# Performance work log

Measured on AMD Instinct MI355X. Metric: run time of the kernel, lower is better.

Reference implementation:

```python
import jax, jax.numpy as jnp
import numpy as np

B, D, T = 8, 256, 8192
N_Q, BINS = 8, 1024
COMMIT_W = 0.25

def setup_inputs() -> dict:
    key = jax.random.key(0)
    k1, k2 = jax.random.split(key)
    x = jax.random.normal(k1, (B, D, T), dtype=jnp.float32)
    codebooks = jax.random.normal(k2, (N_Q, BINS, D), dtype=jnp.float32)
    return {"x": x, "sample_rate": 16000, "codebooks": codebooks}

def _rvq(x_btd, codebooks):
    # x_btd: [B, T, D]; codebooks: [n_q, bins, D]
    def step(residual, cb):
        # nearest codebook entry under squared euclidean distance
        dots = jnp.einsum('btd,kd->btk', residual, cb)          # [B, T, K]
        cb_sq = jnp.sum(cb * cb, axis=-1)                        # [K]
        dist = cb_sq[None, None, :] - 2.0 * dots                 # argmin-equivalent distance
        idx = jnp.argmin(dist, axis=-1)                          # [B, T] int32
        q = cb[idx]                                              # [B, T, D] gather
        # commitment loss (codebook side detached, EnCodec style)
        loss = COMMIT_W * jnp.mean((jax.lax.stop_gradient(q) - residual) ** 2)
        # straight-through estimator
        q_ste = residual + jax.lax.stop_gradient(q - residual)
        return residual - q_ste, (q_ste, idx, loss)

    _, (qs, codes, losses) = jax.lax.scan(step, x_btd, codebooks)
    quantized = jnp.sum(qs, axis=0)                              # [B, T, D]
    return quantized, codes, losses

def reference(x, sample_rate, codebooks):
    n_q = codebooks.shape[0]
    bins = codebooks.shape[1]
    x_btd = jnp.transpose(x, (0, 2, 1))                          # [B, T, D]
    quantized_btd, codes, losses = _rvq(x_btd, codebooks)
    quantized = jnp.transpose(quantized_btd, (0, 2, 1))          # [B, D, T]
    bw_per_q = np.log2(bins) * sample_rate / 1000.0
    bw = jnp.asarray(n_q * bw_per_q, dtype=x.dtype)
    commit_loss = jnp.mean(losses)
    return quantized, codes, bw, commit_loss
```

## Files before the change

kernel.cpp:

```cpp
#include <hip/hip_runtime.h>
#include <math.h>

typedef _Float16 f16;
typedef f16 f16x8 __attribute__((ext_vector_type(8)));
typedef float f32x4 __attribute__((ext_vector_type(4)));

#define B_ 8
#define D_ 256
#define T_ 8192
#define NQ 8
#define KB 1024
#define TT 64
#define NTHR 512

#define OUT_CODES (B_ * D_ * T_)
#define OUT_BW (OUT_CODES + NQ * B_ * T_)
#define OUT_LOSS (OUT_BW + 1)

#define R_BYTES 65536
#define RED_OFF R_BYTES
#define REDI_OFF (RED_OFF + 2048)
#define WSUM_OFF (REDI_OFF + 2048)
#define LDS_TOTAL (WSUM_OFF + 32)

#define WS_HI (8192 * 4)
#define CBW_HALVES (NQ * 8 * KB * 32)
#define WS_LO (WS_HI + CBW_HALVES * 2)

#define MFMA16(a, b, c) __builtin_amdgcn_mfma_f32_16x16x32_f16(a, b, c, 0, 0, 0)

__global__ void init_cbsq_kernel(const float* __restrict__ cb, const int* __restrict__ sr,
                                 float* __restrict__ csq, float* __restrict__ out) {
    int gid = blockIdx.x * blockDim.x + threadIdx.x;
    int row = gid >> 6;
    int lane = gid & 63;
    float4 v = ((const float4*)(cb + (size_t)row * D_))[lane];
    float s = fmaf(v.x, v.x, fmaf(v.y, v.y, fmaf(v.z, v.z, v.w * v.w)));
#pragma unroll
    for (int off = 32; off; off >>= 1) s += __shfl_down(s, off);
    if (lane == 0) csq[row] = s;
    if (gid == 0) {
        out[OUT_BW] = (float)(*sr) * (80.0f / 1000.0f);
        out[OUT_LOSS] = 0.0f;
    }
}

__global__ void init_split_kernel(const float* __restrict__ cb, f16* __restrict__ whi,
                                  f16* __restrict__ wlo) {
    int gid = blockIdx.x * 256 + threadIdx.x;
    int qdc = gid >> 10, k = gid & 1023;
    int q = qdc >> 3, dc = qdc & 7;
    const float* src = cb + ((size_t)(q * 1024 + k)) * 256 + dc * 32;
    size_t wo = (size_t)gid * 32;
#pragma unroll
    for (int jj = 0; jj < 4; ++jj) {
        float4 a = ((const float4*)src)[jj * 2];
        float4 c = ((const float4*)src)[jj * 2 + 1];
        float vals[8] = {a.x, a.y, a.z, a.w, c.x, c.y, c.z, c.w};
        f16x8 hv, lv;
#pragma unroll
        for (int i = 0; i < 8; ++i) {
            f16 h = (f16)vals[i];
            hv[i] = h;
            lv[i] = (f16)(vals[i] - (float)h);
        }
        *(f16x8*)&whi[wo + jj * 8] = hv;
        *(f16x8*)&wlo[wo + jj * 8] = lv;
    }
}

extern "C" __global__ __launch_bounds__(NTHR, 4)
void rvq_kernel(const float* __restrict__ x, const float* __restrict__ cb,
                const float* __restrict__ csq, const f16* __restrict__ whi,
                const f16* __restrict__ wlo, float* __restrict__ out) {
    extern __shared__ char smem[];
    f16* rs = (f16*)smem;
    float* redv = (float*)(smem + RED_OFF);
    int* redi = (int*)(smem + REDI_OFF);
    float* wsum = (float*)(smem + WSUM_OFF);

    const int tid = threadIdx.x;
    const int w = tid >> 6;
    const int l = tid & 63;
    const int l15 = l & 15;
    const int q4 = l >> 4;

    const int b = blockIdx.x >> 7;
    const int t0 = (blockIdx.x & 127) * TT;
    const float* xb = x + (size_t)b * D_ * T_;

    for (int d = tid >> 6; d < D_; d += 8) {
        float v = xb[(size_t)d * T_ + t0 + l];
        f16 h = (f16)v;
        const int sw = l & 7;
        rs[l * 512 + (((d >> 3) ^ sw) << 3) + (d & 7)] = h;
        rs[l * 512 + ((((d >> 3) + 32) ^ sw) << 3) + (d & 7)] = (f16)(v - (float)h);
    }

    float ssq = 0.0f;

    const f16* a_base = rs + l15 * 512;
    const int swA = l15 & 7;

    for (int q = 0; q < NQ; ++q) {
        const float* cbq = cb + (size_t)q * KB * D_;
        const char* wq = (const char*)(whi + (size_t)q * 8 * KB * 32);
        const char* lq = (const char*)(wlo + (size_t)q * 8 * KB * 32);

        __syncthreads();

        float bval[16];
        unsigned bidxp[8];
#pragma unroll
        for (int e = 0; e < 16; ++e) bval[e] = INFINITY;
#pragma unroll
        for (int p = 0; p < 8; ++p) bidxp[p] = 0;

#pragma unroll 1
        for (int s = 0; s < 4; ++s) {
            const int code0 = s * 256 + w * 32 + l15;
            const int vb0 = (code0 << 6) + q4 * 16;

            f32x4 ah[4][2];
#pragma unroll
            for (int mt = 0; mt < 4; ++mt)
#pragma unroll
                for (int nt = 0; nt < 2; ++nt) ah[mt][nt] = (f32x4)0.0f;

            f16x8 sa0h, sa0l, sa1h, sa1l;
            f16x8 sb0h, sb0l, sb1h, sb1l;

#define LOADSET(p0h, p0l, p1h, p1l, dcv) { \
            const char* wd_ = wq + (dcv) * 65536; \
            const char* ld_ = lq + (dcv) * 65536; \
            p0h = *(const f16x8*)(wd_ + vb0); \
            p0l = *(const f16x8*)(ld_ + vb0); \
            p1h = *(const f16x8*)(wd_ + vb0 + 1024); \
            p1l = *(const f16x8*)(ld_ + vb0 + 1024); }

#define STEP(dcv, c0h, c0l, c1h, c1l) { \
            const int ga_ = (dcv) * 4 + q4; \
            const int o1_ = (ga_ ^ swA) << 3; \
            const int o2_ = ((ga_ + 32) ^ swA) << 3; \
            f16x8 afa1 = *(const f16x8*)&a_base[o1_]; \
            f16x8 afa2 = *(const f16x8*)&a_base[o2_]; \
            f16x8 afb1 = *(const f16x8*)&a_base[8192 + o1_]; \
            f16x8 afb2 = *(const f16x8*)&a_base[8192 + o2_]; \
            __builtin_amdgcn_s_setprio(1); \
            ah[0][0] = MFMA16(afa1, c0h, ah[0][0]); \
            ah[0][0] = MFMA16(afa2, c0h, ah[0][0]); \
            ah[0][0] = MFMA16(afa1, c0l, ah[0][0]); \
            ah[0][1] = MFMA16(afa1, c1h, ah[0][1]); \
            ah[0][1] = MFMA16(afa2, c1h, ah[0][1]); \
            ah[0][1] = MFMA16(afa1, c1l, ah[0][1]); \
            __builtin_amdgcn_sched_barrier(0); \
            afa1 = *(const f16x8*)&a_base[16384 + o1_]; \
            afa2 = *(const f16x8*)&a_base[16384 + o2_]; \
            ah[1][0] = MFMA16(afb1, c0h, ah[1][0]); \
            ah[1][0] = MFMA16(afb2, c0h, ah[1][0]); \
            ah[1][0] = MFMA16(afb1, c0l, ah[1][0]); \
            ah[1][1] = MFMA16(afb1, c1h, ah[1][1]); \
            ah[1][1] = MFMA16(afb2, c1h, ah[1][1]); \
            ah[1][1] = MFMA16(afb1, c1l, ah[1][1]); \
            __builtin_amdgcn_sched_barrier(0); \
            afb1 = *(const f16x8*)&a_base[24576 + o1_]; \
            afb2 = *(const f16x8*)&a_base[24576 + o2_]; \
            ah[2][0] = MFMA16(afa1, c0h, ah[2][0]); \
            ah[2][0] = MFMA16(afa2, c0h, ah[2][0]); \
            ah[2][0] = MFMA16(afa1, c0l, ah[2][0]); \
            ah[2][1] = MFMA16(afa1, c1h, ah[2][1]); \
            ah[2][1] = MFMA16(afa2, c1h, ah[2][1]); \
            ah[2][1] = MFMA16(afa1, c1l, ah[2][1]); \
            __builtin_amdgcn_sched_barrier(0); \
            ah[3][0] = MFMA16(afb1, c0h, ah[3][0]); \
            ah[3][0] = MFMA16(afb2, c0h, ah[3][0]); \
            ah[3][0] = MFMA16(afb1, c0l, ah[3][0]); \
            ah[3][1] = MFMA16(afb1, c1h, ah[3][1]); \
            ah[3][1] = MFMA16(afb2, c1h, ah[3][1]); \
            ah[3][1] = MFMA16(afb1, c1l, ah[3][1]); \
            __builtin_amdgcn_s_setprio(0); \
            __builtin_amdgcn_sched_barrier(0); }

            LOADSET(sa0h, sa0l, sa1h, sa1l, 0)
            LOADSET(sb0h, sb0l, sb1h, sb1l, 1)
#pragma unroll 1
            for (int dc2 = 0; dc2 < 6; dc2 += 2) {
                STEP(dc2, sa0h, sa0l, sa1h, sa1l)
                LOADSET(sa0h, sa0l, sa1h, sa1l, dc2 + 2)
                STEP(dc2 + 1, sb0h, sb0l, sb1h, sb1l)
                LOADSET(sb0h, sb0l, sb1h, sb1l, dc2 + 3)
            }
            STEP(6, sa0h, sa0l, sa1h, sa1l)
            STEP(7, sb0h, sb0l, sb1h, sb1l)
#undef LOADSET
#undef STEP

            const float cq0 = csq[q * KB + code0];
            const float cq1 = csq[q * KB + code0 + 16];
#pragma unroll
            for (int nt = 0; nt < 2; ++nt) {
                const int code = code0 + nt * 16;
                const float cq = nt ? cq1 : cq0;
#pragma unroll
                for (int mt = 0; mt < 4; ++mt)
#pragma unroll
                    for (int rg = 0; rg < 4; ++rg) {
                        const int e = mt * 4 + rg;
                        const float dist = fmaf(-2.0f, ah[mt][nt][rg], cq);
                        if (dist < bval[e]) {
                            bval[e] = dist;
                            const int sh = (e & 1) * 16;
                            bidxp[e >> 1] = (bidxp[e >> 1] & ~(0xFFFFu << sh)) |
                                            ((unsigned)code << sh);
                        }
                    }
            }
        }
#pragma unroll
        for (int m = 1; m < 16; m <<= 1) {
#pragma unroll
            for (int p = 0; p < 8; ++p) {
                const unsigned op = __shfl_xor((int)bidxp[p], m);
#pragma unroll
                for (int h = 0; h < 2; ++h) {
                    const int e = p * 2 + h;
                    const float ov = __shfl_xor(bval[e], m);
                    const int sh = h * 16;
                    const unsigned oc = (op >> sh) & 0xFFFFu;
                    const unsigned mc = (bidxp[p] >> sh) & 0xFFFFu;
                    if (ov < bval[e] || (ov == bval[e] && oc < mc)) {
                        bval[e] = ov;
                        bidxp[p] = (bidxp[p] & ~(0xFFFFu << sh)) | (oc << sh);
                    }
                }
            }
        }
        if (l15 == 0) {
#pragma unroll
            for (int mt = 0; mt < 4; ++mt)
#pragma unroll
                for (int rg = 0; rg < 4; ++rg) {
                    const int e = mt * 4 + rg;
                    const int t = mt * 16 + q4 * 4 + rg;
                    redv[w * 64 + t] = bval[e];
                    redi[w * 64 + t] = (int)((bidxp[e >> 1] >> ((e & 1) * 16)) & 0xFFFFu);
                }
        }
        __syncthreads();
        {
            const int t = tid & 63, ch = tid >> 6;
            float bv = redv[t];
            int bi = redi[t];
#pragma unroll
            for (int w2 = 1; w2 < 8; ++w2) {
                const float v = redv[w2 * 64 + t];
                const int ii = redi[w2 * 64 + t];
                if (v < bv || (v == bv && ii < bi)) { bv = v; bi = ii; }
            }
            if (ch == 0) out[OUT_CODES + ((size_t)q * B_ + b) * T_ + t0 + t] = (float)bi;
            const float* crow = cbq + (size_t)bi * D_ + ch * 32;
            f16* rowp = rs + t * 512;
            const int sw = t & 7;
#pragma unroll
            for (int jj = 0; jj < 4; ++jj) {
                const int g = ch * 4 + jj;
                const int g1 = (g ^ sw) << 3;
                const int g2 = ((g + 32) ^ sw) << 3;
                f16x8 hv = *(const f16x8*)&rowp[g1];
                f16x8 lv = *(const f16x8*)&rowp[g2];
                const float4 c0 = ((const float4*)crow)[jj * 2];
                const float4 c1 = ((const float4*)crow)[jj * 2 + 1];
                const float cc[8] = {c0.x, c0.y, c0.z, c0.w, c1.x, c1.y, c1.z, c1.w};
                f16x8 nh, nl;
#pragma unroll
                for (int i = 0; i < 8; ++i) {
                    const float r = (float)hv[i] + (float)lv[i];
                    const float nv = r - cc[i];
                    ssq = fmaf(nv, nv, ssq);
                    const f16 h = (f16)nv;
                    nh[i] = h;
                    nl[i] = (f16)(nv - (float)h);
                }
                *(f16x8*)&rowp[g1] = nh;
                *(f16x8*)&rowp[g2] = nl;
            }
        }
    }
    __syncthreads();
    {
        float* outq = out + (size_t)b * D_ * T_;
        for (int d = tid >> 6; d < D_; d += 8) {
            const int sw = l & 7;
            const float h1 = (float)rs[l * 512 + (((d >> 3) ^ sw) << 3) + (d & 7)];
            const float h2 = (float)rs[l * 512 + ((((d >> 3) + 32) ^ sw) << 3) + (d & 7)];
            const size_t gi = (size_t)d * T_ + t0 + l;
            outq[gi] = xb[gi] - (h1 + h2);
        }
    }
#pragma unroll
    for (int off = 32; off; off >>= 1) ssq += __shfl_down(ssq, off);
    if (l == 0) wsum[w] = ssq;
    __syncthreads();
    if (tid == 0) {
        float tot = 0.0f;
#pragma unroll
        for (int i = 0; i < 8; ++i) tot += wsum[i];
        const float scale = 0.25f / ((float)NQ * (float)B_ * (float)D_ * (float)T_);
        atomicAdd(out + OUT_LOSS, tot * scale);
    }
}

extern "C" void kernel_launch(void* const* d_in, const int* in_sizes, int n_in,
                              void* d_out, int out_size, void* d_ws, size_t ws_size,
                              hipStream_t stream) {
    const float* x = (const float*)d_in[0];
    const int* sr = (const int*)d_in[1];
    const float* cb = (const float*)d_in[2];
    float* out = (float*)d_out;
    float* csq = (float*)d_ws;
    f16* whi = (f16*)((char*)d_ws + WS_HI);
    f16* wlo = (f16*)((char*)d_ws + WS_LO);

    hipFuncSetAttribute((const void*)rvq_kernel, hipFuncAttributeMaxDynamicSharedMemorySize,
                        LDS_TOTAL);

    init_cbsq_kernel<<<2048, 256, 0, stream>>>(cb, sr, csq, out);
    init_split_kernel<<<256, 256, 0, stream>>>(cb, whi, wlo);
    rvq_kernel<<<B_ * (T_ / TT), NTHR, LDS_TOTAL, stream>>>(x, cb, csq, whi, wlo, out);
}
```

Baseline: 976.7 us.

## Prefetch codebook fragments across chunks and use DPP for argmin butterfly

The first two codebook fragment sets are now loaded before the per-codebook barrier. At the end of each 256-code chunk, the next chunk's first fragments are issued while the last MFMA steps of the current chunk run. This hides global-load latency at chunk boundaries and at codebook changes that was previously exposed. The 16-lane argmin reduction swaps shfl_xor for DPP moves (quad_perm, then row_ror by 4 and 8), which avoids LDS-routed shuffles. The cost is higher register pressure from live prefetched fragments and the fully unrolled inner loop.

```diff
diff --git a/kernel.cpp b/kernel.cpp
--- a/kernel.cpp
+++ b/kernel.cpp
@@ -101,12 +101,28 @@
 
     const f16* a_base = rs + l15 * 512;
     const int swA = l15 & 7;
+    const int vb_s0 = ((w * 32 + l15) << 6) + q4 * 16;
 
     for (int q = 0; q < NQ; ++q) {
         const float* cbq = cb + (size_t)q * KB * D_;
         const char* wq = (const char*)(whi + (size_t)q * 8 * KB * 32);
         const char* lq = (const char*)(wlo + (size_t)q * 8 * KB * 32);
 
+        f16x8 sa0h, sa0l, sa1h, sa1l;
+        f16x8 sb0h, sb0l, sb1h, sb1l;
+
+#define LOADSET(p0h, p0l, p1h, p1l, dcv, vbv) { \
+            const char* wd_ = wq + (dcv) * 65536; \
+            const char* ld_ = lq + (dcv) * 65536; \
+            p0h = *(const f16x8*)(wd_ + (vbv)); \
+            p0l = *(const f16x8*)(ld_ + (vbv)); \
+            p1h = *(const f16x8*)(wd_ + (vbv) + 1024); \
+            p1l = *(const f16x8*)(ld_ + (vbv) + 1024); }
+
+        int vb = vb_s0;
+        LOADSET(sa0h, sa0l, sa1h, sa1l, 0, vb)
+        LOADSET(sb0h, sb0l, sb1h, sb1l, 1, vb)
+
         __syncthreads();
 
         float bval[16];
@@ -115,28 +131,6 @@
         for (int e = 0; e < 16; ++e) bval[e] = INFINITY;
 #pragma unroll
         for (int p = 0; p < 8; ++p) bidxp[p] = 0;
-
-#pragma unroll 1
-        for (int s = 0; s < 4; ++s) {
-            const int code0 = s * 256 + w * 32 + l15;
-            const int vb0 = (code0 << 6) + q4 * 16;
-
-            f32x4 ah[4][2];
-#pragma unroll
-            for (int mt = 0; mt < 4; ++mt)
-#pragma unroll
-                for (int nt = 0; nt < 2; ++nt) ah[mt][nt] = (f32x4)0.0f;
-
-            f16x8 sa0h, sa0l, sa1h, sa1l;
-            f16x8 sb0h, sb0l, sb1h, sb1l;
-
-#define LOADSET(p0h, p0l, p1h, p1l, dcv) { \
-            const char* wd_ = wq + (dcv) * 65536; \
-            const char* ld_ = lq + (dcv) * 65536; \
-            p0h = *(const f16x8*)(wd_ + vb0); \
-            p0l = *(const f16x8*)(ld_ + vb0); \
-            p1h = *(const f16x8*)(wd_ + vb0 + 1024); \
-            p1l = *(const f16x8*)(ld_ + vb0 + 1024); }
 
 #define STEP(dcv, c0h, c0l, c1h, c1l) { \
             const int ga_ = (dcv) * 4 + q4; \
@@ -181,22 +175,32 @@
             __builtin_amdgcn_s_setprio(0); \
             __builtin_amdgcn_sched_barrier(0); }
 
-            LOADSET(sa0h, sa0l, sa1h, sa1l, 0)
-            LOADSET(sb0h, sb0l, sb1h, sb1l, 1)
 #pragma unroll 1
+        for (int s = 0; s < 4; ++s) {
+            const int code0 = s * 256 + w * 32 + l15;
+            const float cq0 = csq[q * KB + code0];
+            const float cq1 = csq[q * KB + code0 + 16];
+
+            f32x4 ah[4][2];
+#pragma unroll
+            for (int mt = 0; mt < 4; ++mt)
+#pragma unroll
+                for (int nt = 0; nt < 2; ++nt) ah[mt][nt] = (f32x4)0.0f;
+
+#pragma unroll
             for (int dc2 = 0; dc2 < 6; dc2 += 2) {
                 STEP(dc2, sa0h, sa0l, sa1h, sa1l)
-                LOADSET(sa0h, sa0l, sa1h, sa1l, dc2 + 2)
+                LOADSET(sa0h, sa0l, sa1h, sa1l, dc2 + 2, vb)
                 STEP(dc2 + 1, sb0h, sb0l, sb1h, sb1l)
-                LOADSET(sb0h, sb0l, sb1h, sb1l, dc2 + 3)
+                LOADSET(sb0h, sb0l, sb1h, sb1l, dc2 + 3, vb)
             }
             STEP(6, sa0h, sa0l, sa1h, sa1l)
+            const int vbn = vb + 16384;
+            if (s < 3) { LOADSET(sa0h, sa0l, sa1h, sa1l, 0, vbn) }
             STEP(7, sb0h, sb0l, sb1h, sb1l)
-#undef LOADSET
-#undef STEP
-
-            const float cq0 = csq[q * KB + code0];
-            const float cq1 = csq[q * KB + code0 + 16];
+            if (s < 3) { LOADSET(sb0h, sb0l, sb1h, sb1l, 1, vbn) }
+            vb = vbn;
+
 #pragma unroll
             for (int nt = 0; nt < 2; ++nt) {
                 const int code = code0 + nt * 16;
@@ -216,25 +220,30 @@
                     }
             }
         }
-#pragma unroll
-        for (int m = 1; m < 16; m <<= 1) {
-#pragma unroll
-            for (int p = 0; p < 8; ++p) {
-                const unsigned op = __shfl_xor((int)bidxp[p], m);
-#pragma unroll
-                for (int h = 0; h < 2; ++h) {
-                    const int e = p * 2 + h;
-                    const float ov = __shfl_xor(bval[e], m);
-                    const int sh = h * 16;
-                    const unsigned oc = (op >> sh) & 0xFFFFu;
-                    const unsigned mc = (bidxp[p] >> sh) & 0xFFFFu;
-                    if (ov < bval[e] || (ov == bval[e] && oc < mc)) {
-                        bval[e] = ov;
-                        bidxp[p] = (bidxp[p] & ~(0xFFFFu << sh)) | (oc << sh);
-                    }
-                }
-            }
-        }
+#undef STEP
+#undef LOADSET
+
+#define BFLY(CTRL) { \
+        _Pragma("unroll") \
+        for (int p = 0; p < 8; ++p) { \
+            const unsigned op = (unsigned)__builtin_amdgcn_mov_dpp((int)bidxp[p], CTRL, 0xF, 0xF, false); \
+            _Pragma("unroll") \
+            for (int h = 0; h < 2; ++h) { \
+                const int e = p * 2 + h; \
+                const float ov = __int_as_float(__builtin_amdgcn_mov_dpp(__float_as_int(bval[e]), CTRL, 0xF, 0xF, false)); \
+                const int sh = h * 16; \
+                const unsigned oc = (op >> sh) & 0xFFFFu; \
+                const unsigned mc = (bidxp[p] >> sh) & 0xFFFFu; \
+                if (ov < bval[e] || (ov == bval[e] && oc < mc)) { \
+                    bval[e] = ov; \
+                    bidxp[p] = (bidxp[p] & ~(0xFFFFu << sh)) | (oc << sh); \
+                } } } }
+        BFLY(0xB1)
+        BFLY(0x4E)
+        BFLY(0x124)
+        BFLY(0x128)
+#undef BFLY
+
         if (l15 == 0) {
 #pragma unroll
             for (int mt = 0; mt < 4; ++mt)
```

After: 1.038 ms. 1.06x slower.
